# Kernel optimization log

Hardware: AMD Instinct MI355X
Metric: run time of the kernel (lower is better)

Reference implementation:

```python
import jax, jax.numpy as jnp
import numpy as np

USER_NUM = 100000
ITEM_NUM = 50000
E = 128   # embedding_size
A = 64    # attention_size
M = 8     # memory_size
B = 4096  # batch
NF = 50   # friends per user


def _l2norm(x, axis):
    # torch F.normalize(p=2): x / max(||x||, eps)
    n = jnp.sqrt(jnp.sum(x * x, axis=axis, keepdims=True))
    return x / jnp.maximum(n, 1e-12)


def setup_inputs() -> dict:
    key = jax.random.key(0)
    ks = jax.random.split(key, 9)
    u = lambda k, shape: jax.random.uniform(k, shape, jnp.float32, -0.1, 0.1)
    return {
        "input_u": jax.random.randint(ks[0], (B,), 0, USER_NUM),
        "input_i": jax.random.randint(ks[1], (B,), 0, ITEM_NUM),
        "input_uf": jax.random.randint(ks[2], (B, NF), 0, USER_NUM + 1),
        "uidW": u(ks[3], (USER_NUM + 1, E)),
        "iidW": u(ks[4], (ITEM_NUM, E)),
        "i_bias": jnp.zeros((ITEM_NUM,), jnp.float32),
        "Key": u(ks[5], (E, M)),
        "Mem": jnp.ones((M, E), jnp.float32),
        "WA": u(ks[6], (E, A)),
        "BA": jnp.zeros((A,), jnp.float32),
        "U_omega": u(ks[7], (A, 1)),
    }


def reference(input_u, input_i, input_uf, uidW, iidW, i_bias, Key, Mem, WA, BA, U_omega):
    user_num = uidW.shape[0] - 1  # padding id
    uid = uidW[input_u]                      # [B, E]
    iid = iidW[input_i]                      # [B, E]
    i_b = i_bias[input_i]                    # [B]
    fe = uidW[input_uf]                      # [B, F, E] friend embeddings
    fn = (input_uf != user_num).astype(uid.dtype)  # [B, F] valid-friend mask

    fe = fn[:, :, None] * fe
    uid_n = _l2norm(uid, axis=1)
    fe_n = _l2norm(fe, axis=2)
    cross = uid_n[:, None, :] * fe_n                     # [B, F, E]
    att_key = jnp.einsum('bfe,em->bfm', cross, Key)      # [B, F, M]
    att_mem = jax.nn.softmax(att_key, axis=0)            # softmax over batch (faithful to dim=0)
    att_mem = fn[:, :, None] * att_mem
    f1 = jnp.einsum('bfm,me->bfe', att_mem, Mem)         # [B, F, E]
    f2 = f1 * fe
    h = jax.nn.relu(jnp.einsum('bfe,ea->bfa', f2, WA) + BA)
    j = jnp.exp(jnp.einsum('bfa,ao->bfo', h, U_omega))   # [B, F, 1]
    j = fn[:, :, None] * j
    w = j / (jnp.sum(j, axis=1, keepdims=True) + 1e-8)
    friend = jnp.sum(w * f2, axis=1)                     # [B, E] (dropout p=0 -> identity)
    user = uid + friend
    score = jnp.sum(user * iid, axis=1) + i_b            # [B]
    return score
```

## Files before the change

### kernel.cpp

```cpp
#include <hip/hip_runtime.h>

#define EDIM 128
#define MDIM 8
#define ADIM 64
#define NFR  50
#define NCOL (NFR * MDIM)
#define NSLICE 64

typedef __attribute__((ext_vector_type(8))) short short8;
typedef __attribute__((ext_vector_type(4))) float f32x4;

__device__ __forceinline__ float waveReduceSum(float v) {
    #pragma unroll
    for (int s = 32; s >= 1; s >>= 1) v += __shfl_xor(v, s, 64);
    return v;
}
__device__ __forceinline__ short f2bf(float x) {
    unsigned u = __float_as_uint(x);
    u += 0x7FFFu + ((u >> 16) & 1u);
    return (short)(u >> 16);
}
__device__ __forceinline__ float bf2f(short s) {
    return __uint_as_float(((unsigned)(unsigned short)s) << 16);
}
__device__ __forceinline__ int fragOff(int r, int e) {
    int q = (e >> 3) & 3;
    int slot = (q * 16 + (r & 15)) ^ (q << 1);
    int block = ((r >> 4) << 2) | (e >> 5);
    return (block * 64 + slot) * 8;
}
__device__ __forceinline__ int slotR(int l) { return l ^ (((l >> 4) & 3) << 1); }

__global__ __launch_bounds__(256)
void k0_prep(const float* __restrict__ WA, const float* __restrict__ Key,
             short* __restrict__ WAfrag, short* __restrict__ Keyfrag,
             float* __restrict__ Ssum)
{
    int t = blockIdx.x * 256 + threadIdx.x;
    for (int i = t; i < NSLICE * NCOL; i += 5 * 256) Ssum[i] = 0.f;
    if (t < 1024) {
        int lane = t & 63;
        int Kt = (t >> 6) & 3;
        int Nt = t >> 8;
        int n  = Nt * 16 + (lane & 15);
        int k0 = Kt * 32 + (lane >> 4) * 8;
        short8 v;
        #pragma unroll
        for (int j = 0; j < 8; ++j) v[j] = f2bf(WA[(size_t)(k0 + j) * ADIM + n]);
        *(short8*)(WAfrag + (size_t)t * 8) = v;
    } else if (t < 1280) {
        int i = t - 1024;
        int lane = i & 63;
        int Kt = i >> 6;
        int n  = lane & 15;
        int k0 = Kt * 32 + (lane >> 4) * 8;
        short8 v;
        #pragma unroll
        for (int j = 0; j < 8; ++j)
            v[j] = (n < MDIM) ? f2bf(Key[(size_t)(k0 + j) * MDIM + n]) : (short)0;
        *(short8*)(Keyfrag + (size_t)i * 8) = v;
    }
}

__global__ __launch_bounds__(256, 4)
void k1_attkey(const int* __restrict__ input_u, const int* __restrict__ input_uf,
               const float* __restrict__ uidW, const short* __restrict__ Keyfrag,
               float* __restrict__ att_key, short* __restrict__ feW,
               float* __restrict__ Ssum, int user_num)
{
    const int b = blockIdx.x, t = threadIdx.x, w = t >> 6, l = t & 63;
    __shared__ short crossF[64 * EDIM];
    __shared__ float uidnL[EDIM];
    __shared__ float redW[4];
    __shared__ int ufL[64];

    const int u = input_u[b];
    float x = (t < EDIM) ? uidW[(size_t)u * EDIM + t] : 0.f;
    float s = waveReduceSum(x * x);
    if (l == 0) redW[w] = s;
    if (t < NFR) ufL[t] = input_uf[(size_t)b * NFR + t];
    else if (t < 64) ufL[t] = user_num;
    __syncthreads();
    float uinv = 1.0f / fmaxf(sqrtf(redW[0] + redW[1] + redW[2] + redW[3]), 1e-12f);
    if (t < EDIM) uidnL[t] = x * uinv;
    __syncthreads();

    const int kg = t & 15, fl = t >> 4;
    const int e0 = kg * 8;
    float4 un0 = *(const float4*)&uidnL[e0];
    float4 un1 = *(const float4*)&uidnL[e0 + 4];

    #pragma unroll
    for (int it = 0; it < 4; ++it) {
        int f = fl + 16 * it;
        short8 outv = {0, 0, 0, 0, 0, 0, 0, 0};
        if (f < NFR) {
            int fid = ufL[f];
            float fn = (fid != user_num) ? 1.f : 0.f;
            const float* fp = uidW + (size_t)fid * EDIM + e0;
            float4 g0 = *(const float4*)fp;
            float4 g1 = *(const float4*)(fp + 4);
            g0.x *= fn; g0.y *= fn; g0.z *= fn; g0.w *= fn;
            g1.x *= fn; g1.y *= fn; g1.z *= fn; g1.w *= fn;
            short8 fev;
            fev[0] = f2bf(g0.x); fev[1] = f2bf(g0.y);
            fev[2] = f2bf(g0.z); fev[3] = f2bf(g0.w);
            fev[4] = f2bf(g1.x); fev[5] = f2bf(g1.y);
            fev[6] = f2bf(g1.z); fev[7] = f2bf(g1.w);
            *(short8*)(feW + ((size_t)b * NFR + f) * EDIM + e0) = fev;
            float fss = g0.x*g0.x + g0.y*g0.y + g0.z*g0.z + g0.w*g0.w
                      + g1.x*g1.x + g1.y*g1.y + g1.z*g1.z + g1.w*g1.w;
            fss += __shfl_xor(fss, 1, 64);
            fss += __shfl_xor(fss, 2, 64);
            fss += __shfl_xor(fss, 4, 64);
            fss += __shfl_xor(fss, 8, 64);
            float inv = 1.0f / fmaxf(sqrtf(fss), 1e-12f);
            outv[0] = f2bf(un0.x * g0.x * inv);
            outv[1] = f2bf(un0.y * g0.y * inv);
            outv[2] = f2bf(un0.z * g0.z * inv);
            outv[3] = f2bf(un0.w * g0.w * inv);
            outv[4] = f2bf(un1.x * g1.x * inv);
            outv[5] = f2bf(un1.y * g1.y * inv);
            outv[6] = f2bf(un1.z * g1.z * inv);
            outv[7] = f2bf(un1.w * g1.w * inv);
        }
        *(short8*)&crossF[fragOff(f, e0)] = outv;
    }
    __syncthreads();

    f32x4 acc = {0.f, 0.f, 0.f, 0.f};
    const int sl = slotR(l);
    #pragma unroll
    for (int Kt = 0; Kt < 4; ++Kt) {
        short8 a  = *(const short8*)&crossF[(((w << 2) | Kt) * 64 + sl) * 8];
        short8 bf = *(const short8*)(Keyfrag + (size_t)((Kt * 64 + l)) * 8);
        acc = __builtin_amdgcn_mfma_f32_16x16x32_bf16(a, bf, acc, 0, 0, 0);
    }
    const int m = l & 15;
    if (m < MDIM) {
        float* Ss = Ssum + (size_t)(b & (NSLICE - 1)) * NCOL;
        const int fbase = w * 16 + (l >> 4) * 4;
        #pragma unroll
        for (int r = 0; r < 4; ++r) {
            int f = fbase + r;
            if (f < NFR) {
                att_key[((size_t)b * NFR + f) * MDIM + m] = acc[r];
                atomicAdd(&Ss[f * MDIM + m], __expf(acc[r]));
            }
        }
    }
}

__global__ __launch_bounds__(256)
void k2b_merge(const float* __restrict__ Ssum, float* __restrict__ ise)
{
    int col = blockIdx.x * 256 + threadIdx.x;
    if (col >= NCOL) return;
    float S = 0.f;
    #pragma unroll
    for (int s = 0; s < NSLICE; ++s) S += Ssum[s * NCOL + col];
    ise[col] = 1.0f / S;
}

__global__ __launch_bounds__(256, 4)
void k3_final(const int* __restrict__ input_u, const int* __restrict__ input_i,
              const int* __restrict__ input_uf, const float* __restrict__ uidW,
              const float* __restrict__ iidW, const float* __restrict__ i_bias,
              const float* __restrict__ Mem, const short* __restrict__ WAfrag,
              const float* __restrict__ BA, const float* __restrict__ U_omega,
              const float* __restrict__ att_key, const short* __restrict__ feW,
              const float* __restrict__ ise, float* __restrict__ out,
              int user_num)
{
    const int b = blockIdx.x, t = threadIdx.x, w = t >> 6, l = t & 63;
    __shared__ short f2F[64 * EDIM];
    __shared__ float amL[NCOL];
    __shared__ int ufL[64];
    __shared__ float pPart[4 * 64];
    __shared__ float jxL[64];
    __shared__ float accW[4][EDIM];
    __shared__ float red2[2];
    __shared__ float wsS;

    if (t < NFR) ufL[t] = input_uf[(size_t)b * NFR + t];
    else if (t < 64) ufL[t] = user_num;
    __syncthreads();

    for (int i = t; i < NCOL; i += 256) {
        float ak = att_key[(size_t)b * NCOL + i];
        amL[i] = (ufL[i >> 3] != user_num) ? __expf(ak) * ise[i] : 0.f;
    }

    const int kg = t & 15, fl = t >> 4;
    const int e0 = kg * 8;
    float4 mA[MDIM], mB[MDIM];
    #pragma unroll
    for (int m = 0; m < MDIM; ++m) {
        mA[m] = *(const float4*)&Mem[m * EDIM + e0];
        mB[m] = *(const float4*)&Mem[m * EDIM + e0 + 4];
    }
    __syncthreads();

    #pragma unroll
    for (int it = 0; it < 4; ++it) {
        int f = fl + 16 * it;
        short8 outv = {0, 0, 0, 0, 0, 0, 0, 0};
        if (f < NFR) {
            short8 fv = *(const short8*)(feW + ((size_t)b * NFR + f) * EDIM + e0);
            float4 am0 = *(const float4*)&amL[f * 8];
            float4 am1 = *(const float4*)&amL[f * 8 + 4];
            float4 fa = {0.f, 0.f, 0.f, 0.f}, fb = {0.f, 0.f, 0.f, 0.f};
            #pragma unroll
            for (int m = 0; m < 4; ++m) {
                float c0 = (&am0.x)[m], c1 = (&am1.x)[m];
                fa.x += c0 * mA[m].x + c1 * mA[m + 4].x;
                fa.y += c0 * mA[m].y + c1 * mA[m + 4].y;
                fa.z += c0 * mA[m].z + c1 * mA[m + 4].z;
                fa.w += c0 * mA[m].w + c1 * mA[m + 4].w;
                fb.x += c0 * mB[m].x + c1 * mB[m + 4].x;
                fb.y += c0 * mB[m].y + c1 * mB[m + 4].y;
                fb.z += c0 * mB[m].z + c1 * mB[m + 4].z;
                fb.w += c0 * mB[m].w + c1 * mB[m + 4].w;
            }
            outv[0] = f2bf(fa.x * bf2f(fv[0]));
            outv[1] = f2bf(fa.y * bf2f(fv[1]));
            outv[2] = f2bf(fa.z * bf2f(fv[2]));
            outv[3] = f2bf(fa.w * bf2f(fv[3]));
            outv[4] = f2bf(fb.x * bf2f(fv[4]));
            outv[5] = f2bf(fb.y * bf2f(fv[5]));
            outv[6] = f2bf(fb.z * bf2f(fv[6]));
            outv[7] = f2bf(fb.w * bf2f(fv[7]));
        }
        *(short8*)&f2F[fragOff(f, e0)] = outv;
    }
    __syncthreads();

    const int sl = slotR(l);
    f32x4 acc[4];
    #pragma unroll
    for (int Mt = 0; Mt < 4; ++Mt) acc[Mt] = (f32x4){0.f, 0.f, 0.f, 0.f};
    #pragma unroll
    for (int Kt = 0; Kt < 4; ++Kt) {
        short8 bf = *(const short8*)(WAfrag + (size_t)(((w << 2) | Kt) * 64 + l) * 8);
        #pragma unroll
        for (int Mt = 0; Mt < 4; ++Mt) {
            short8 a = *(const short8*)&f2F[(((Mt << 2) | Kt) * 64 + sl) * 8];
            acc[Mt] = __builtin_amdgcn_mfma_f32_16x16x32_bf16(a, bf, acc[Mt], 0, 0, 0);
        }
    }

    const int aIdx = w * 16 + (l & 15);
    const float ba = BA[aIdx];
    const float uo = U_omega[aIdx];
    float v[16];
    #pragma unroll
    for (int Mt = 0; Mt < 4; ++Mt)
        #pragma unroll
        for (int r = 0; r < 4; ++r)
            v[Mt * 4 + r] = fmaxf(acc[Mt][r] + ba, 0.f) * uo;

    const bool c0 = l & 1, c1 = l & 2, c2 = l & 4, c3 = l & 8;
    #pragma unroll
    for (int k = 0; k < 8; ++k) {
        float lo = v[k], hi = v[k + 8];
        float send = c0 ? lo : hi;
        float recv = __shfl_xor(send, 1, 64);
        v[k] = c0 ? (hi + recv) : (lo + recv);
    }
    #pragma unroll
    for (int k = 0; k < 4; ++k) {
        float lo = v[k], hi = v[k + 4];
        float send = c1 ? lo : hi;
        float recv = __shfl_xor(send, 2, 64);
        v[k] = c1 ? (hi + recv) : (lo + recv);
    }
    #pragma unroll
    for (int k = 0; k < 2; ++k) {
        float lo = v[k], hi = v[k + 2];
        float send = c2 ? lo : hi;
        float recv = __shfl_xor(send, 4, 64);
        v[k] = c2 ? (hi + recv) : (lo + recv);
    }
    {
        float lo = v[0], hi = v[1];
        float send = c3 ? lo : hi;
        float recv = __shfl_xor(send, 8, 64);
        v[0] = c3 ? (hi + recv) : (lo + recv);
    }
    const int vIdx = ((l & 1) << 3) | ((l & 2) << 1) | ((l & 4) >> 1) | ((l & 8) >> 3);
    const int fLane = (vIdx >> 2) * 16 + (l >> 4) * 4 + (vIdx & 3);
    pPart[w * 64 + fLane] = v[0];
    __syncthreads();

    if (t < 64) {
        float p = pPart[t] + pPart[64 + t] + pPart[128 + t] + pPart[192 + t];
        float jv = 0.f;
        if (t < NFR && ufL[t] != user_num) jv = __expf(p);
        jxL[t] = jv;
        float wsum = waveReduceSum(jv);
        if (t == 0) wsS = wsum + 1e-8f;
    }
    __syncthreads();

    float pa[8] = {0.f, 0.f, 0.f, 0.f, 0.f, 0.f, 0.f, 0.f};
    #pragma unroll
    for (int it = 0; it < 4; ++it) {
        int f = fl + 16 * it;
        float jf = jxL[f];
        short8 vv = *(const short8*)&f2F[fragOff(f, e0)];
        #pragma unroll
        for (int j = 0; j < 8; ++j) pa[j] += jf * bf2f(vv[j]);
    }
    #pragma unroll
    for (int j = 0; j < 8; ++j) {
        pa[j] += __shfl_xor(pa[j], 16, 64);
        pa[j] += __shfl_xor(pa[j], 32, 64);
    }
    if (l < 16) {
        #pragma unroll
        for (int j = 0; j < 8; ++j) accW[w][l * 8 + j] = pa[j];
    }
    __syncthreads();

    if (t < EDIM) {
        const float winv = 1.0f / wsS;
        float fr = (accW[0][t] + accW[1][t] + accW[2][t] + accW[3][t]) * winv;
        const int u = input_u[b];
        const int ii = input_i[b];
        float sc = (uidW[(size_t)u * EDIM + t] + fr) * iidW[(size_t)ii * EDIM + t];
        float p = waveReduceSum(sc);
        if ((t & 63) == 0) red2[t >> 6] = p;
    }
    __syncthreads();
    if (t == 0) out[b] = red2[0] + red2[1] + i_bias[input_i[b]];
}

extern "C" void kernel_launch(void* const* d_in, const int* in_sizes, int n_in,
                              void* d_out, int out_size, void* d_ws, size_t ws_size,
                              hipStream_t stream)
{
    const int*   input_u  = (const int*)d_in[0];
    const int*   input_i  = (const int*)d_in[1];
    const int*   input_uf = (const int*)d_in[2];
    const float* uidW     = (const float*)d_in[3];
    const float* iidW     = (const float*)d_in[4];
    const float* i_bias   = (const float*)d_in[5];
    const float* Key      = (const float*)d_in[6];
    const float* Mem      = (const float*)d_in[7];
    const float* WA       = (const float*)d_in[8];
    const float* BA       = (const float*)d_in[9];
    const float* U_om     = (const float*)d_in[10];

    const int B = in_sizes[0];
    const int user_num = in_sizes[3] / EDIM - 1;

    float* att  = (float*)d_ws;
    float* Ssum = att + (size_t)B * NCOL;
    float* ise  = Ssum + NSLICE * NCOL;
    short* WAfrag  = (short*)(ise + NCOL);
    short* Keyfrag = WAfrag + 4 * 4 * 64 * 8;
    short* feW     = Keyfrag + 4 * 64 * 8;

    k0_prep<<<5, 256, 0, stream>>>(WA, Key, WAfrag, Keyfrag, Ssum);
    k1_attkey<<<B, 256, 0, stream>>>(input_u, input_uf, uidW, Keyfrag, att, feW,
                                     Ssum, user_num);
    k2b_merge<<<2, 256, 0, stream>>>(Ssum, ise);
    k3_final<<<B, 256, 0, stream>>>(input_u, input_i, input_uf, uidW, iidW, i_bias,
                                    Mem, WAfrag, BA, U_om, att, feW, ise,
                                    (float*)d_out, user_num);
}
```

Measured before the change: 187.1 us.

## Map one batch row per wavefront and regather friend embeddings instead of feW

Both main kernels now give each wavefront a whole batch row, four rows per block. Block-wide __syncthreads and shared-memory reductions become wave barriers and shuffles, and each wave issues all MFMA tiles for its row. The bf16 friend-embedding buffer feW is no longer written in k1 and read in k3. k3 instead regathers the fp32 friend rows from uidW, trading a workspace round trip for a second random gather. Per-block shared memory grows about fourfold and the occupancy hint drops to 2, which may reduce latency hiding.

```diff
diff --git a/kernel.cpp b/kernel.cpp
--- a/kernel.cpp
+++ b/kernel.cpp
@@ -62,52 +62,47 @@
     }
 }
 
-__global__ __launch_bounds__(256, 4)
+__global__ __launch_bounds__(256, 2)
 void k1_attkey(const int* __restrict__ input_u, const int* __restrict__ input_uf,
                const float* __restrict__ uidW, const short* __restrict__ Keyfrag,
-               float* __restrict__ att_key, short* __restrict__ feW,
-               float* __restrict__ Ssum, int user_num)
-{
-    const int b = blockIdx.x, t = threadIdx.x, w = t >> 6, l = t & 63;
-    __shared__ short crossF[64 * EDIM];
-    __shared__ float uidnL[EDIM];
-    __shared__ float redW[4];
-    __shared__ int ufL[64];
+               float* __restrict__ att_key, float* __restrict__ Ssum,
+               int user_num, int B)
+{
+    __shared__ short crossF4[4][64 * EDIM];
+    __shared__ float uidn4[4][EDIM];
+    const int w = threadIdx.x >> 6, l = threadIdx.x & 63;
+    const int b = blockIdx.x * 4 + w;
+    if (b >= B) return;
+    short* cF = crossF4[w];
+    float* uidn = uidn4[w];
 
     const int u = input_u[b];
-    float x = (t < EDIM) ? uidW[(size_t)u * EDIM + t] : 0.f;
-    float s = waveReduceSum(x * x);
-    if (l == 0) redW[w] = s;
-    if (t < NFR) ufL[t] = input_uf[(size_t)b * NFR + t];
-    else if (t < 64) ufL[t] = user_num;
-    __syncthreads();
-    float uinv = 1.0f / fmaxf(sqrtf(redW[0] + redW[1] + redW[2] + redW[3]), 1e-12f);
-    if (t < EDIM) uidnL[t] = x * uinv;
-    __syncthreads();
-
-    const int kg = t & 15, fl = t >> 4;
+    int ufv = (l < NFR) ? input_uf[(size_t)b * NFR + l] : user_num;
+    float x0 = uidW[(size_t)u * EDIM + l];
+    float x1 = uidW[(size_t)u * EDIM + 64 + l];
+    float s = waveReduceSum(x0 * x0 + x1 * x1);
+    float uinv = 1.0f / fmaxf(sqrtf(s), 1e-12f);
+    uidn[l] = x0 * uinv;
+    uidn[64 + l] = x1 * uinv;
+    __builtin_amdgcn_wave_barrier();
+
+    const int kg = l & 15, fl = l >> 4;
     const int e0 = kg * 8;
-    float4 un0 = *(const float4*)&uidnL[e0];
-    float4 un1 = *(const float4*)&uidnL[e0 + 4];
-
-    #pragma unroll
-    for (int it = 0; it < 4; ++it) {
-        int f = fl + 16 * it;
+    float4 un0 = *(const float4*)&uidn[e0];
+    float4 un1 = *(const float4*)&uidn[e0 + 4];
+
+    #pragma unroll 4
+    for (int it = 0; it < 13; ++it) {
+        int f = fl + 4 * it;
         short8 outv = {0, 0, 0, 0, 0, 0, 0, 0};
         if (f < NFR) {
-            int fid = ufL[f];
+            int fid = __shfl(ufv, f, 64);
             float fn = (fid != user_num) ? 1.f : 0.f;
             const float* fp = uidW + (size_t)fid * EDIM + e0;
             float4 g0 = *(const float4*)fp;
             float4 g1 = *(const float4*)(fp + 4);
             g0.x *= fn; g0.y *= fn; g0.z *= fn; g0.w *= fn;
             g1.x *= fn; g1.y *= fn; g1.z *= fn; g1.w *= fn;
-            short8 fev;
-            fev[0] = f2bf(g0.x); fev[1] = f2bf(g0.y);
-            fev[2] = f2bf(g0.z); fev[3] = f2bf(g0.w);
-            fev[4] = f2bf(g1.x); fev[5] = f2bf(g1.y);
-            fev[6] = f2bf(g1.z); fev[7] = f2bf(g1.w);
-            *(short8*)(feW + ((size_t)b * NFR + f) * EDIM + e0) = fev;
             float fss = g0.x*g0.x + g0.y*g0.y + g0.z*g0.z + g0.w*g0.w
                       + g1.x*g1.x + g1.y*g1.y + g1.z*g1.z + g1.w*g1.w;
             fss += __shfl_xor(fss, 1, 64);
@@ -124,28 +119,36 @@
             outv[6] = f2bf(un1.z * g1.z * inv);
             outv[7] = f2bf(un1.w * g1.w * inv);
         }
-        *(short8*)&crossF[fragOff(f, e0)] = outv;
-    }
-    __syncthreads();
-
-    f32x4 acc = {0.f, 0.f, 0.f, 0.f};
+        *(short8*)&cF[fragOff(f, e0)] = outv;
+    }
+    __builtin_amdgcn_wave_barrier();
+
     const int sl = slotR(l);
+    f32x4 acc[4];
+    #pragma unroll
+    for (int Mt = 0; Mt < 4; ++Mt) acc[Mt] = (f32x4){0.f, 0.f, 0.f, 0.f};
     #pragma unroll
     for (int Kt = 0; Kt < 4; ++Kt) {
-        short8 a  = *(const short8*)&crossF[(((w << 2) | Kt) * 64 + sl) * 8];
-        short8 bf = *(const short8*)(Keyfrag + (size_t)((Kt * 64 + l)) * 8);
-        acc = __builtin_amdgcn_mfma_f32_16x16x32_bf16(a, bf, acc, 0, 0, 0);
+        short8 bf = *(const short8*)(Keyfrag + (size_t)(Kt * 64 + l) * 8);
+        #pragma unroll
+        for (int Mt = 0; Mt < 4; ++Mt) {
+            short8 a = *(const short8*)&cF[(((Mt << 2) | Kt) * 64 + sl) * 8];
+            acc[Mt] = __builtin_amdgcn_mfma_f32_16x16x32_bf16(a, bf, acc[Mt], 0, 0, 0);
+        }
     }
     const int m = l & 15;
     if (m < MDIM) {
         float* Ss = Ssum + (size_t)(b & (NSLICE - 1)) * NCOL;
-        const int fbase = w * 16 + (l >> 4) * 4;
-        #pragma unroll
-        for (int r = 0; r < 4; ++r) {
-            int f = fbase + r;
-            if (f < NFR) {
-                att_key[((size_t)b * NFR + f) * MDIM + m] = acc[r];
-                atomicAdd(&Ss[f * MDIM + m], __expf(acc[r]));
+        #pragma unroll
+        for (int Mt = 0; Mt < 4; ++Mt) {
+            const int fbase = Mt * 16 + (l >> 4) * 4;
+            #pragma unroll
+            for (int r = 0; r < 4; ++r) {
+                int f = fbase + r;
+                if (f < NFR) {
+                    att_key[((size_t)b * NFR + f) * MDIM + m] = acc[Mt][r];
+                    atomicAdd(&Ss[f * MDIM + m], __expf(acc[Mt][r]));
+                }
             }
         }
     }
@@ -162,51 +165,60 @@
     ise[col] = 1.0f / S;
 }
 
-__global__ __launch_bounds__(256, 4)
+__global__ __launch_bounds__(256, 2)
 void k3_final(const int* __restrict__ input_u, const int* __restrict__ input_i,
               const int* __restrict__ input_uf, const float* __restrict__ uidW,
               const float* __restrict__ iidW, const float* __restrict__ i_bias,
               const float* __restrict__ Mem, const short* __restrict__ WAfrag,
               const float* __restrict__ BA, const float* __restrict__ U_omega,
-              const float* __restrict__ att_key, const short* __restrict__ feW,
-              const float* __restrict__ ise, float* __restrict__ out,
-              int user_num)
-{
-    const int b = blockIdx.x, t = threadIdx.x, w = t >> 6, l = t & 63;
-    __shared__ short f2F[64 * EDIM];
-    __shared__ float amL[NCOL];
-    __shared__ int ufL[64];
-    __shared__ float pPart[4 * 64];
-    __shared__ float jxL[64];
-    __shared__ float accW[4][EDIM];
-    __shared__ float red2[2];
-    __shared__ float wsS;
-
-    if (t < NFR) ufL[t] = input_uf[(size_t)b * NFR + t];
-    else if (t < 64) ufL[t] = user_num;
-    __syncthreads();
-
-    for (int i = t; i < NCOL; i += 256) {
-        float ak = att_key[(size_t)b * NCOL + i];
-        amL[i] = (ufL[i >> 3] != user_num) ? __expf(ak) * ise[i] : 0.f;
-    }
-
-    const int kg = t & 15, fl = t >> 4;
+              const float* __restrict__ att_key, const float* __restrict__ ise,
+              float* __restrict__ out, int user_num, int B)
+{
+    __shared__ short f2F4[4][64 * EDIM];
+    __shared__ float amL4[4][NCOL];
+    __shared__ float jxL4[4][64];
+    const int w = threadIdx.x >> 6, l = threadIdx.x & 63;
+    const int b = blockIdx.x * 4 + w;
+    if (b >= B) return;
+    short* f2F = f2F4[w];
+    float* amL = amL4[w];
+    float* jxL = jxL4[w];
+
+    const int u = input_u[b];
+    const int ii = input_i[b];
+    const float ib = i_bias[ii];
+    int ufv = (l < NFR) ? input_uf[(size_t)b * NFR + l] : user_num;
+
+    const int kg = l & 15, fl = l >> 4;
     const int e0 = kg * 8;
+
+    #pragma unroll
+    for (int c = 0; c < 7; ++c) {
+        int i = l + 64 * c;
+        if (i < NCOL) {
+            float ak = att_key[(size_t)b * NCOL + i];
+            int fid = __shfl(ufv, i >> 3, 64);
+            amL[i] = (fid != user_num) ? __expf(ak) * ise[i] : 0.f;
+        }
+    }
+
     float4 mA[MDIM], mB[MDIM];
     #pragma unroll
     for (int m = 0; m < MDIM; ++m) {
         mA[m] = *(const float4*)&Mem[m * EDIM + e0];
         mB[m] = *(const float4*)&Mem[m * EDIM + e0 + 4];
     }
-    __syncthreads();
-
-    #pragma unroll
-    for (int it = 0; it < 4; ++it) {
-        int f = fl + 16 * it;
+    __builtin_amdgcn_wave_barrier();
+
+    #pragma unroll 4
+    for (int it = 0; it < 16; ++it) {
+        int f = fl + 4 * it;
         short8 outv = {0, 0, 0, 0, 0, 0, 0, 0};
         if (f < NFR) {
-            short8 fv = *(const short8*)(feW + ((size_t)b * NFR + f) * EDIM + e0);
+            int fid = __shfl(ufv, f, 64);
+            const float* fp = uidW + (size_t)fid * EDIM + e0;
+            float4 g0 = *(const float4*)fp;
+            float4 g1 = *(const float4*)(fp + 4);
             float4 am0 = *(const float4*)&amL[f * 8];
             float4 am1 = *(const float4*)&amL[f * 8 + 4];
             float4 fa = {0.f, 0.f, 0.f, 0.f}, fb = {0.f, 0.f, 0.f, 0.f};
@@ -222,42 +234,57 @@
                 fb.z += c0 * mB[m].z + c1 * mB[m + 4].z;
                 fb.w += c0 * mB[m].w + c1 * mB[m + 4].w;
             }
-            outv[0] = f2bf(fa.x * bf2f(fv[0]));
-            outv[1] = f2bf(fa.y * bf2f(fv[1]));
-            outv[2] = f2bf(fa.z * bf2f(fv[2]));
-            outv[3] = f2bf(fa.w * bf2f(fv[3]));
-            outv[4] = f2bf(fb.x * bf2f(fv[4]));
-            outv[5] = f2bf(fb.y * bf2f(fv[5]));
-            outv[6] = f2bf(fb.z * bf2f(fv[6]));
-            outv[7] = f2bf(fb.w * bf2f(fv[7]));
+            outv[0] = f2bf(fa.x * g0.x);
+            outv[1] = f2bf(fa.y * g0.y);
+            outv[2] = f2bf(fa.z * g0.z);
+            outv[3] = f2bf(fa.w * g0.w);
+            outv[4] = f2bf(fb.x * g1.x);
+            outv[5] = f2bf(fb.y * g1.y);
+            outv[6] = f2bf(fb.z * g1.z);
+            outv[7] = f2bf(fb.w * g1.w);
         }
         *(short8*)&f2F[fragOff(f, e0)] = outv;
     }
-    __syncthreads();
+    __builtin_amdgcn_wave_barrier();
 
     const int sl = slotR(l);
-    f32x4 acc[4];
-    #pragma unroll
-    for (int Mt = 0; Mt < 4; ++Mt) acc[Mt] = (f32x4){0.f, 0.f, 0.f, 0.f};
+    f32x4 acc[4][4];
+    #pragma unroll
+    for (int Mt = 0; Mt < 4; ++Mt)
+        #pragma unroll
+        for (int Nt = 0; Nt < 4; ++Nt) acc[Mt][Nt] = (f32x4){0.f, 0.f, 0.f, 0.f};
     #pragma unroll
     for (int Kt = 0; Kt < 4; ++Kt) {
-        short8 bf = *(const short8*)(WAfrag + (size_t)(((w << 2) | Kt) * 64 + l) * 8);
-        #pragma unroll
-        for (int Mt = 0; Mt < 4; ++Mt) {
-            short8 a = *(const short8*)&f2F[(((Mt << 2) | Kt) * 64 + sl) * 8];
-            acc[Mt] = __builtin_amdgcn_mfma_f32_16x16x32_bf16(a, bf, acc[Mt], 0, 0, 0);
-        }
-    }
-
-    const int aIdx = w * 16 + (l & 15);
-    const float ba = BA[aIdx];
-    const float uo = U_omega[aIdx];
+        short8 a[4];
+        #pragma unroll
+        for (int Mt = 0; Mt < 4; ++Mt)
+            a[Mt] = *(const short8*)&f2F[(((Mt << 2) | Kt) * 64 + sl) * 8];
+        #pragma unroll
+        for (int Nt = 0; Nt < 4; ++Nt) {
+            short8 bf = *(const short8*)(WAfrag + (size_t)(((Nt << 2) | Kt) * 64 + l) * 8);
+            #pragma unroll
+            for (int Mt = 0; Mt < 4; ++Mt)
+                acc[Mt][Nt] = __builtin_amdgcn_mfma_f32_16x16x32_bf16(a[Mt], bf, acc[Mt][Nt], 0, 0, 0);
+        }
+    }
+
+    float ba4[4], uo4[4];
+    #pragma unroll
+    for (int Nt = 0; Nt < 4; ++Nt) {
+        ba4[Nt] = BA[Nt * 16 + kg];
+        uo4[Nt] = U_omega[Nt * 16 + kg];
+    }
     float v[16];
     #pragma unroll
     for (int Mt = 0; Mt < 4; ++Mt)
         #pragma unroll
-        for (int r = 0; r < 4; ++r)
-            v[Mt * 4 + r] = fmaxf(acc[Mt][r] + ba, 0.f) * uo;
+        for (int r = 0; r < 4; ++r) {
+            float sv = 0.f;
+            #pragma unroll
+            for (int Nt = 0; Nt < 4; ++Nt)
+                sv += fmaxf(acc[Mt][Nt][r] + ba4[Nt], 0.f) * uo4[Nt];
+            v[Mt * 4 + r] = sv;
+        }
 
     const bool c0 = l & 1, c1 = l & 2, c2 = l & 4, c3 = l & 8;
     #pragma unroll
@@ -289,23 +316,18 @@
     }
     const int vIdx = ((l & 1) << 3) | ((l & 2) << 1) | ((l & 4) >> 1) | ((l & 8) >> 3);
     const int fLane = (vIdx >> 2) * 16 + (l >> 4) * 4 + (vIdx & 3);
-    pPart[w * 64 + fLane] = v[0];
-    __syncthreads();
-
-    if (t < 64) {
-        float p = pPart[t] + pPart[64 + t] + pPart[128 + t] + pPart[192 + t];
-        float jv = 0.f;
-        if (t < NFR && ufL[t] != user_num) jv = __expf(p);
-        jxL[t] = jv;
-        float wsum = waveReduceSum(jv);
-        if (t == 0) wsS = wsum + 1e-8f;
-    }
-    __syncthreads();
+
+    int ufF = __shfl(ufv, fLane, 64);
+    float jv = 0.f;
+    if (fLane < NFR && ufF != user_num) jv = __expf(v[0]);
+    jxL[fLane] = jv;
+    float winv = 1.0f / (waveReduceSum(jv) + 1e-8f);
+    __builtin_amdgcn_wave_barrier();
 
     float pa[8] = {0.f, 0.f, 0.f, 0.f, 0.f, 0.f, 0.f, 0.f};
-    #pragma unroll
-    for (int it = 0; it < 4; ++it) {
-        int f = fl + 16 * it;
+    #pragma unroll 4
+    for (int it = 0; it < 16; ++it) {
+        int f = fl + 4 * it;
         float jf = jxL[f];
         short8 vv = *(const short8*)&f2F[fragOff(f, e0)];
         #pragma unroll
@@ -316,23 +338,21 @@
         pa[j] += __shfl_xor(pa[j], 16, 64);
         pa[j] += __shfl_xor(pa[j], 32, 64);
     }
-    if (l < 16) {
-        #pragma unroll
-        for (int j = 0; j < 8; ++j) accW[w][l * 8 + j] = pa[j];
-    }
-    __syncthreads();
-
-    if (t < EDIM) {
-        const float winv = 1.0f / wsS;
-        float fr = (accW[0][t] + accW[1][t] + accW[2][t] + accW[3][t]) * winv;
-        const int u = input_u[b];
-        const int ii = input_i[b];
-        float sc = (uidW[(size_t)u * EDIM + t] + fr) * iidW[(size_t)ii * EDIM + t];
-        float p = waveReduceSum(sc);
-        if ((t & 63) == 0) red2[t >> 6] = p;
-    }
-    __syncthreads();
-    if (t == 0) out[b] = red2[0] + red2[1] + i_bias[input_i[b]];
+
+    const float* up = uidW + (size_t)u * EDIM + e0;
+    const float* ip = iidW + (size_t)ii * EDIM + e0;
+    float4 u0 = *(const float4*)up;
+    float4 u1 = *(const float4*)(up + 4);
+    float4 i0 = *(const float4*)ip;
+    float4 i1 = *(const float4*)(ip + 4);
+    float sc = 0.f;
+    #pragma unroll
+    for (int j = 0; j < 4; ++j) {
+        sc += ((&u0.x)[j] + pa[j] * winv) * (&i0.x)[j];
+        sc += ((&u1.x)[j] + pa[j + 4] * winv) * (&i1.x)[j];
+    }
+    float red = waveReduceSum(sc);
+    if (l == 0) out[b] = red * 0.25f + ib;
 }
 
 extern "C" void kernel_launch(void* const* d_in, const int* in_sizes, int n_in,
@@ -359,13 +379,13 @@
     float* ise  = Ssum + NSLICE * NCOL;
     short* WAfrag  = (short*)(ise + NCOL);
     short* Keyfrag = WAfrag + 4 * 4 * 64 * 8;
-    short* feW     = Keyfrag + 4 * 64 * 8;
-
+
+    const int nb = (B + 3) / 4;
     k0_prep<<<5, 256, 0, stream>>>(WA, Key, WAfrag, Keyfrag, Ssum);
-    k1_attkey<<<B, 256, 0, stream>>>(input_u, input_uf, uidW, Keyfrag, att, feW,
-                                     Ssum, user_num);
+    k1_attkey<<<nb, 256, 0, stream>>>(input_u, input_uf, uidW, Keyfrag, att,
+                                      Ssum, user_num, B);
     k2b_merge<<<2, 256, 0, stream>>>(Ssum, ise);
-    k3_final<<<B, 256, 0, stream>>>(input_u, input_i, input_uf, uidW, iidW, i_bias,
-                                    Mem, WAfrag, BA, U_om, att, feW, ise,
-                                    (float*)d_out, user_num);
-}
+    k3_final<<<nb, 256, 0, stream>>>(input_u, input_i, input_uf, uidW, iidW, i_bias,
+                                     Mem, WAfrag, BA, U_om, att, ise,
+                                     (float*)d_out, user_num, B);
+}
```

Measured after the change: 173.0 us. 7.6% less time.
